# Performance work log

Hardware: AMD Instinct MI355X
Metric: run time of the kernel (lower is better)

The kernel has to match this reference:

```python
import jax, jax.numpy as jnp
import numpy as np

N = 50000
E = 800000
IN_DIM = 128
HID = 32
HEADS = 8
OUT_DIM = 2
NEG_SLOPE = 0.2


def setup_inputs() -> dict:
    key = jax.random.key(0)
    ks = jax.random.split(key, 10)
    x = jax.random.normal(ks[0], (N, IN_DIM), dtype=jnp.float32)
    edge_index = jax.random.randint(ks[1], (2, E), 0, N, dtype=jnp.int64)
    s = 0.1
    W1 = jax.random.normal(ks[2], (IN_DIM, HEADS * HID), dtype=jnp.float32) * s
    att_src1 = jax.random.normal(ks[3], (HEADS, HID), dtype=jnp.float32) * s
    att_dst1 = jax.random.normal(ks[4], (HEADS, HID), dtype=jnp.float32) * s
    b1 = jnp.zeros((HEADS * HID,), dtype=jnp.float32)
    W2 = jax.random.normal(ks[5], (HEADS * HID, OUT_DIM), dtype=jnp.float32) * s
    att_src2 = jax.random.normal(ks[6], (1, OUT_DIM), dtype=jnp.float32) * s
    att_dst2 = jax.random.normal(ks[7], (1, OUT_DIM), dtype=jnp.float32) * s
    b2 = jnp.zeros((OUT_DIM,), dtype=jnp.float32)
    return {"x": x, "edge_index": edge_index, "W1": W1, "att_src1": att_src1,
            "att_dst1": att_dst1, "b1": b1, "W2": W2, "att_src2": att_src2,
            "att_dst2": att_dst2, "b2": b2}


def gat_conv(x, src, dst, W, att_src, att_dst, bias, concat):
    # PyG GATConv (add_self_loops handled by caller already appended in src/dst)
    H, C = att_src.shape
    n = x.shape[0]
    h = (x @ W).reshape(n, H, C)                       # [N,H,C]
    a_src = jnp.einsum('nhc,hc->nh', h, att_src)       # [N,H]
    a_dst = jnp.einsum('nhc,hc->nh', h, att_dst)       # [N,H]
    e = jax.nn.leaky_relu(a_src[src] + a_dst[dst], NEG_SLOPE)  # [Etot,H]
    m = jax.lax.stop_gradient(jax.ops.segment_max(e, dst, num_segments=n))
    ee = jnp.exp(e - m[dst])
    denom = jax.ops.segment_sum(ee, dst, num_segments=n)
    alpha = ee / denom[dst]                            # segment softmax over incoming edges
    out = jax.ops.segment_sum(alpha[:, :, None] * h[src], dst, num_segments=n)  # [N,H,C]
    if concat:
        out = out.reshape(n, H * C)
    else:
        out = out.mean(axis=1)
    return out + bias


def reference(x, edge_index, W1, att_src1, att_dst1, b1, W2, att_src2, att_dst2, b2):
    n = x.shape[0]
    loop = jnp.arange(n, dtype=edge_index.dtype)
    src = jnp.concatenate([edge_index[0], loop])
    dst = jnp.concatenate([edge_index[1], loop])
    h = gat_conv(x, src, dst, W1, att_src1, att_dst1, b1, concat=True)
    h = jax.nn.elu(h)
    # dropout inactive in eval mode
    h = gat_conv(h, src, dst, W2, att_src2, att_dst2, b2, concat=False)
    return jax.nn.log_softmax(h, axis=1)
```

## Files before the change

### kernel.cpp

```cpp
#include <hip/hip_runtime.h>
#include <hip/hip_bf16.h>

#define NEG_SLOPE 0.2f
#define BSTRIDE 6144

typedef float f32x4 __attribute__((ext_vector_type(4)));
typedef short s16x4 __attribute__((ext_vector_type(4)));
typedef short bf16x8 __attribute__((ext_vector_type(8)));

__device__ __forceinline__ float lrelu(float x) { return x > 0.f ? x : NEG_SLOPE * x; }
__device__ __forceinline__ float bf2f(unsigned u) {
    return __uint_as_float(u << 16);
}
__device__ __forceinline__ unsigned short f2bf(float f) {
    unsigned int u = __float_as_uint(f);
    return (unsigned short)((u + 0x7FFF + ((u >> 16) & 1)) >> 16);
}

__device__ __forceinline__ int load_src(const int* ei, int E, int e, int is64) {
    return is64 ? ei[2 * (size_t)e] : ei[e];
}
__device__ __forceinline__ int load_dst(const int* ei, int E, int e, int is64) {
    return is64 ? ei[2 * (size_t)E + 2 * (size_t)e] : ei[(size_t)E + e];
}

__global__ void init2_kernel(const int* __restrict__ ei, int* __restrict__ flag,
                             int* __restrict__ bktCur) {
    int t = threadIdx.x;
    bktCur[t] = t * BSTRIDE;
    if (t == 0) {
        int z = 1;
        for (int k = 0; k < 64; ++k) if (ei[2 * k + 1] != 0) { z = 0; break; }
        *flag = z;
    }
}

__global__ __launch_bounds__(256) void bin_scatter(const int* __restrict__ ei, int E, int n,
                                                   const int* __restrict__ flag,
                                                   int* __restrict__ bktCur,
                                                   int* __restrict__ binned) {
    __shared__ int hist[256];
    __shared__ int gb[256];
    int t = threadIdx.x;
    hist[t] = 0;
    __syncthreads();
    int is64 = *flag;
    int base = blockIdx.x * 2048;
    int Etot = E + n;
    int rec[8], rb[8], rr[8];
#pragma unroll
    for (int k = 0; k < 8; ++k) {
        int e = base + k * 256 + t;
        rb[k] = -1;
        if (e < Etot) {
            int s, d;
            if (e < E) { s = load_src(ei, E, e, is64); d = load_dst(ei, E, e, is64); }
            else       { s = d = e - E; }
            int b = d >> 8;
            rb[k] = b;
            rec[k] = s | ((d & 255) << 24);
            rr[k] = atomicAdd(&hist[b], 1);
        }
    }
    __syncthreads();
    if (hist[t]) gb[t] = atomicAdd(&bktCur[t], hist[t]);
    __syncthreads();
#pragma unroll
    for (int k = 0; k < 8; ++k)
        if (rb[k] >= 0) binned[gb[rb[k]] + rr[k]] = rec[k];
}

__global__ __launch_bounds__(256) void bucket_build(const int* __restrict__ bktCur,
                                                    const int* __restrict__ binned,
                                                    int* __restrict__ offs,
                                                    int* __restrict__ degOut,
                                                    int* __restrict__ csr, int n) {
    __shared__ int deg[256];
    __shared__ int sd[256];
    int b = blockIdx.x;
    int t = threadIdx.x;
    int lo = b * BSTRIDE, hi = bktCur[b];
    deg[t] = 0;
    __syncthreads();
    for (int i = lo + t; i < hi; i += 256)
        atomicAdd(&deg[((unsigned)binned[i]) >> 24], 1);
    __syncthreads();
    int v = deg[t];
    sd[t] = v;
    __syncthreads();
    for (int o = 1; o < 256; o <<= 1) {
        int x = (t >= o) ? sd[t - o] : 0;
        __syncthreads();
        sd[t] += x;
        __syncthreads();
    }
    int excl = lo + sd[t] - v;
    int node = (b << 8) + t;
    if (node < n) { offs[node] = excl; degOut[node] = v; }
    __syncthreads();
    deg[t] = excl;
    __syncthreads();
    for (int i = lo + t; i < hi; i += 256) {
        unsigned r = (unsigned)binned[i];
        int pos = atomicAdd(&deg[r >> 24], 1);
        csr[pos] = (int)(r & 0xFFFFFF);
    }
}

__global__ __launch_bounds__(256) void w1prep_kernel(
        const float* __restrict__ W1, const float* __restrict__ att_src1,
        const float* __restrict__ att_dst1, unsigned short* __restrict__ w1t) {
    int t = threadIdx.x;
    if (blockIdx.x < 128) {
        int v = blockIdx.x * 256 + t;
        int col = v & 255, k = v >> 8;
        w1t[(size_t)col * 128 + k] = f2bf(W1[(size_t)k * 256 + col]);
    } else {
#pragma unroll
        for (int i = 0; i < 8; ++i) {
            int v = t + 256 * i;
            int j = v & 15, k = v >> 4;
            const float* av = (j < 8) ? att_src1 : att_dst1;
            int h = j & 7;
            float s = 0.f;
            for (int c = 0; c < 32; ++c)
                s += W1[(size_t)k * 256 + 32 * h + c] * av[h * 32 + c];
            w1t[(size_t)(256 + j) * 128 + k] = f2bf(s);
        }
    }
}

__device__ __forceinline__ bf16x8 read_frag(const char* base, int row, int kb) {
    int swz = (row & 7) << 4;
    const char* p = base + row * 256;
    s16x4 lo = *(const s16x4*)(p + (kb ^ swz));
    s16x4 hi = *(const s16x4*)(p + ((kb + 32) ^ swz));
    return __builtin_shufflevector(lo, hi, 0, 1, 2, 3, 4, 5, 6, 7);
}

__device__ __forceinline__ void load_px(const float* __restrict__ x, int m0, int n, int t,
                                        f32x4 (&px)[2][4]) {
#pragma unroll
    for (int q = 0; q < 2; ++q) {
        int u = t + 256 * q;
        int row = u >> 3, kseg = u & 7;
        int gr = m0 + row;
        bool ok = (u < 384) && (gr < n);
        const f32x4* p = (const f32x4*)(x + (size_t)gr * 128 + kseg * 16);
#pragma unroll
        for (int j = 0; j < 4; ++j) {
            f32x4 z = {0.f, 0.f, 0.f, 0.f};
            px[q][j] = ok ? p[j] : z;
        }
    }
}

#define XOFF 69632
__global__ __launch_bounds__(256, 2) void gemm1_kernel(
        const float* __restrict__ x, const unsigned short* __restrict__ w1t,
        unsigned short* __restrict__ h1u, float* __restrict__ asrc1,
        float* __restrict__ adst1, int n, int nchunk) {
    __shared__ __align__(16) char lds[81920];
    const int t = threadIdx.x;
    const int lane = t & 63, w = t >> 6;
    const int l15 = lane & 15, g = lane >> 4;

    for (int u = t; u < 4352; u += 256) {
        int col = u >> 4, seg = u & 15;
        int4 v = *(const int4*)(w1t + (size_t)col * 128 + seg * 8);
        *(int4*)(lds + col * 256 + ((seg * 16) ^ ((col & 7) << 4))) = v;
    }

    int c0 = blockIdx.x * 2;
    f32x4 px[2][4];
    load_px(x, c0 * 48, n, t, px);
    __syncthreads();

    bf16x8 Bf[4][5];
#pragma unroll
    for (int ks = 0; ks < 4; ++ks) {
#pragma unroll
        for (int nt = 0; nt < 5; ++nt) {
            if (nt < 4 || w == 0) {
                int col = (nt < 4) ? (64 * w + 16 * nt + l15) : (256 + l15);
                Bf[ks][nt] = read_frag(lds, col, 64 * ks + 8 * g);
            }
        }
    }

    for (int cc = 0; cc < 2; ++cc) {
        int chunk = c0 + cc;
        if (chunk >= nchunk) break;
        int m0 = chunk * 48;
#pragma unroll
        for (int q = 0; q < 2; ++q) {
            int u = t + 256 * q;
            if (u < 384) {
                int row = u >> 3, kseg = u & 7;
                union { unsigned short us[16]; int4 v[2]; } pk;
#pragma unroll
                for (int j = 0; j < 4; ++j)
#pragma unroll
                    for (int e = 0; e < 4; ++e) pk.us[j * 4 + e] = f2bf(px[q][j][e]);
                int base = XOFF + row * 256;
                int swz = (row & 7) << 4;
                *(int4*)(lds + base + ((kseg * 32) ^ swz)) = pk.v[0];
                *(int4*)(lds + base + ((kseg * 32 + 16) ^ swz)) = pk.v[1];
            }
        }
        __syncthreads();
        if (cc == 0) load_px(x, (c0 + 1) * 48, n, t, px);

        f32x4 acc[3][5];
#pragma unroll
        for (int mt = 0; mt < 3; ++mt)
#pragma unroll
            for (int nt = 0; nt < 5; ++nt)
#pragma unroll
                for (int r = 0; r < 4; ++r) acc[mt][nt][r] = 0.f;

#pragma unroll
        for (int ks = 0; ks < 4; ++ks) {
            bf16x8 Af[3];
#pragma unroll
            for (int mt = 0; mt < 3; ++mt)
                Af[mt] = read_frag(lds + XOFF, mt * 16 + l15, 64 * ks + 8 * g);
#pragma unroll
            for (int nt = 0; nt < 5; ++nt) {
                if (nt < 4 || w == 0) {
#pragma unroll
                    for (int mt = 0; mt < 3; ++mt)
                        acc[mt][nt] = __builtin_amdgcn_mfma_f32_16x16x32_bf16(
                            Af[mt], Bf[ks][nt], acc[mt][nt], 0, 0, 0);
                }
            }
        }

#pragma unroll
        for (int mt = 0; mt < 3; ++mt) {
#pragma unroll
            for (int r = 0; r < 4; ++r) {
                int row = m0 + 16 * mt + 4 * g + r;
                bool ok = row < n;
#pragma unroll
                for (int nt = 0; nt < 4; ++nt)
                    if (ok) h1u[(size_t)row * 256 + 64 * w + 16 * nt + l15] =
                        f2bf(acc[mt][nt][r]);
                if (w == 0 && ok) {
                    float v = acc[mt][4][r];
                    if (l15 < 8) asrc1[(size_t)row * 8 + l15] = v;
                    else         adst1[(size_t)row * 8 + (l15 - 8)] = v;
                }
            }
        }
        if (cc == 0) __syncthreads();
    }
}

__global__ __launch_bounds__(64) void aggregate_kernel(
        const int* __restrict__ offs, const int* __restrict__ deg,
        const int* __restrict__ csr,
        const float* __restrict__ asrc1, const float* __restrict__ adst1,
        const unsigned short* __restrict__ h1u, const float* __restrict__ b1,
        const float* __restrict__ W2, const float* __restrict__ att_src2,
        const float* __restrict__ att_dst2, float4* __restrict__ rec) {
    int d = blockIdx.x;
    int t = threadIdx.x;
    int h = t >> 3;
    int off = offs[d], end = off + deg[d];
    float ad = adst1[(size_t)d * 8 + h];
    float a0 = 0.f, a1 = 0.f, a2 = 0.f, a3 = 0.f, aw = 0.f;
    const unsigned short* hp = h1u + 4 * t;
    int i = off;
    for (; i + 8 <= end; i += 8) {
        int sIdx[8];
#pragma unroll
        for (int k = 0; k < 8; ++k) sIdx[k] = csr[i + k];
        float wv[8];
#pragma unroll
        for (int k = 0; k < 8; ++k)
            wv[k] = __expf(lrelu(asrc1[(size_t)sIdx[k] * 8 + h] + ad));
        ushort4 hv[8];
#pragma unroll
        for (int k = 0; k < 8; ++k)
            hv[k] = *(const ushort4*)(hp + (size_t)sIdx[k] * 256);
#pragma unroll
        for (int k = 0; k < 8; ++k) {
            a0 = fmaf(wv[k], bf2f(hv[k].x), a0);
            a1 = fmaf(wv[k], bf2f(hv[k].y), a1);
            a2 = fmaf(wv[k], bf2f(hv[k].z), a2);
            a3 = fmaf(wv[k], bf2f(hv[k].w), a3);
            aw += wv[k];
        }
    }
    for (; i < end; ++i) {
        int s = csr[i];
        float w = __expf(lrelu(asrc1[(size_t)s * 8 + h] + ad));
        ushort4 v = *(const ushort4*)(hp + (size_t)s * 256);
        a0 = fmaf(w, bf2f(v.x), a0); a1 = fmaf(w, bf2f(v.y), a1);
        a2 = fmaf(w, bf2f(v.z), a2); a3 = fmaf(w, bf2f(v.w), a3);
        aw += w;
    }
    float inv = 1.0f / aw;
    float4 bv = *(const float4*)(b1 + 4 * t);
    float v0 = fmaf(a0, inv, bv.x);
    float v1 = fmaf(a1, inv, bv.y);
    float v2 = fmaf(a2, inv, bv.z);
    float v3 = fmaf(a3, inv, bv.w);
    v0 = v0 > 0.f ? v0 : __expf(v0) - 1.f;
    v1 = v1 > 0.f ? v1 : __expf(v1) - 1.f;
    v2 = v2 > 0.f ? v2 : __expf(v2) - 1.f;
    v3 = v3 > 0.f ? v3 : __expf(v3) - 1.f;
    float4 w01 = *(const float4*)(W2 + 8 * t);
    float4 w23 = *(const float4*)(W2 + 8 * t + 4);
    float p0 = v0 * w01.x + v1 * w01.z + v2 * w23.x + v3 * w23.z;
    float p1 = v0 * w01.y + v1 * w01.w + v2 * w23.y + v3 * w23.w;
#pragma unroll
    for (int o = 32; o; o >>= 1) { p0 += __shfl_down(p0, o); p1 += __shfl_down(p1, o); }
    if (t == 0) {
        float s2a = att_src2[0], s2b = att_src2[1];
        float d2a = att_dst2[0], d2b = att_dst2[1];
        rec[d] = make_float4(p0, p1, p0 * s2a + p1 * s2b, p0 * d2a + p1 * d2b);
    }
}

__global__ __launch_bounds__(256) void layer2_kernel(
        const int* __restrict__ offs, const int* __restrict__ deg,
        const int* __restrict__ csr, const float4* __restrict__ rec,
        const float* __restrict__ b2, float* __restrict__ out, int n) {
    int t = threadIdx.x;
    int d = blockIdx.x * 16 + (t >> 4);
    if (d >= n) return;
    int li = t & 15;
    int off = offs[d], end = off + deg[d];
    float ad = rec[d].w;
    float se = 0.f, s0 = 0.f, s1 = 0.f;
    for (int i = off + li; i < end; i += 16) {
        int s = csr[i];
        float4 r = rec[s];
        float e = __expf(lrelu(r.z + ad));
        se += e;
        s0 = fmaf(e, r.x, s0);
        s1 = fmaf(e, r.y, s1);
    }
#pragma unroll
    for (int o = 8; o; o >>= 1) {
        se += __shfl_xor(se, o, 16);
        s0 += __shfl_xor(s0, o, 16);
        s1 += __shfl_xor(s1, o, 16);
    }
    if (li == 0) {
        float o0 = s0 / se + b2[0];
        float o1 = s1 / se + b2[1];
        float m2 = fmaxf(o0, o1);
        float lse = m2 + logf(__expf(o0 - m2) + __expf(o1 - m2));
        out[(size_t)d * 2 + 0] = o0 - lse;
        out[(size_t)d * 2 + 1] = o1 - lse;
    }
}

extern "C" void kernel_launch(void* const* d_in, const int* in_sizes, int n_in,
                              void* d_out, int out_size, void* d_ws, size_t ws_size,
                              hipStream_t stream) {
    const float* x        = (const float*)d_in[0];
    const int*   ei       = (const int*)d_in[1];
    const float* W1       = (const float*)d_in[2];
    const float* att_src1 = (const float*)d_in[3];
    const float* att_dst1 = (const float*)d_in[4];
    const float* b1       = (const float*)d_in[5];
    const float* W2       = (const float*)d_in[6];
    const float* att_src2 = (const float*)d_in[7];
    const float* att_dst2 = (const float*)d_in[8];
    const float* b2       = (const float*)d_in[9];
    float* out = (float*)d_out;

    int N = in_sizes[0] / 128;
    int E = in_sizes[1] / 2;
    int Etot = E + N;
    int NB = (N + 255) >> 8;
    int nbs = (Etot + 2047) / 2048;
    int nchunk = (N + 47) / 48;
    size_t binsz = (size_t)NB * BSTRIDE;

    char* W = (char*)d_ws;
    size_t o = 0;
    auto alloc = [&](size_t bytes) { size_t r = o; o = (o + bytes + 15) & ~(size_t)15; return r; };
    unsigned short* h1u  = (unsigned short*)(W + alloc((size_t)N * 256 * 2));
    float*  asrc1   = (float*)(W + alloc((size_t)N * 8 * 4));
    float*  adst1   = (float*)(W + alloc((size_t)N * 8 * 4));
    float4* rec     = (float4*)(W + alloc((size_t)N * 16));
    int*    offs    = (int*)(W + alloc((size_t)N * 4));
    int*    deg     = (int*)(W + alloc((size_t)N * 4));
    int*    bktCur  = (int*)(W + alloc(256 * 4));
    int*    flag    = (int*)(W + alloc(16));
    int*    csr     = (int*)(W + alloc(binsz * 4));
    int*    binned  = (int*)(W + alloc(binsz * 4));
    unsigned short* w1t = (unsigned short*)(W + alloc((size_t)272 * 128 * 2));

    init2_kernel<<<1, 256, 0, stream>>>(ei, flag, bktCur);
    bin_scatter<<<nbs, 256, 0, stream>>>(ei, E, N, flag, bktCur, binned);
    bucket_build<<<NB, 256, 0, stream>>>(bktCur, binned, offs, deg, csr, N);
    w1prep_kernel<<<129, 256, 0, stream>>>(W1, att_src1, att_dst1, w1t);
    gemm1_kernel<<<(nchunk + 1) / 2, 256, 0, stream>>>(x, w1t, h1u, asrc1, adst1, N, nchunk);
    aggregate_kernel<<<N, 64, 0, stream>>>(offs, deg, csr, asrc1, adst1, h1u, b1, W2,
                                           att_src2, att_dst2, rec);
    layer2_kernel<<<(N + 15) / 16, 256, 0, stream>>>(offs, deg, csr, rec, b2, out, N);
}
```

Before: 168.4 us.

## Stage GEMM1 output through swizzled LDS for coalesced stores; split aggregate launch

The GEMM1 epilogue now writes the bf16 results into a swizzled LDS tile, synchronises, and then emits 16-byte coalesced row stores to h1u instead of scattered 2-byte global stores. The attention-score writes move into a separate wave-0 loop. Edge-index loading in bin_scatter uses int2 reads for 64-bit indices. The aggregate kernel is also split into two half-size launches with a node offset. The extra barrier and LDS reuse add sync cost, and the split launch adds launch overhead with no obvious benefit.

```diff
diff --git a/kernel.cpp b/kernel.cpp
--- a/kernel.cpp
+++ b/kernel.cpp
@@ -15,13 +15,6 @@
 __device__ __forceinline__ unsigned short f2bf(float f) {
     unsigned int u = __float_as_uint(f);
     return (unsigned short)((u + 0x7FFF + ((u >> 16) & 1)) >> 16);
-}
-
-__device__ __forceinline__ int load_src(const int* ei, int E, int e, int is64) {
-    return is64 ? ei[2 * (size_t)e] : ei[e];
-}
-__device__ __forceinline__ int load_dst(const int* ei, int E, int e, int is64) {
-    return is64 ? ei[2 * (size_t)E + 2 * (size_t)e] : ei[(size_t)E + e];
 }
 
 __global__ void init2_kernel(const int* __restrict__ ei, int* __restrict__ flag,
@@ -54,8 +47,15 @@
         rb[k] = -1;
         if (e < Etot) {
             int s, d;
-            if (e < E) { s = load_src(ei, E, e, is64); d = load_dst(ei, E, e, is64); }
-            else       { s = d = e - E; }
+            if (e < E) {
+                if (is64) {
+                    s = ((const int2*)ei)[e].x;
+                    d = ((const int2*)(ei + 2 * (size_t)E))[e].x;
+                } else {
+                    s = ei[e];
+                    d = ei[(size_t)E + e];
+                }
+            } else { s = d = e - E; }
             int b = d >> 8;
             rb[k] = b;
             rec[k] = s | ((d & 255) << 24);
@@ -236,21 +236,41 @@
             }
         }
 
+        if (w == 0) {
+#pragma unroll
+            for (int mt = 0; mt < 3; ++mt)
+#pragma unroll
+                for (int r = 0; r < 4; ++r) {
+                    int row = m0 + 16 * mt + 4 * g + r;
+                    if (row < n) {
+                        float v = acc[mt][4][r];
+                        if (l15 < 8) asrc1[(size_t)row * 8 + l15] = v;
+                        else         adst1[(size_t)row * 8 + (l15 - 8)] = v;
+                    }
+                }
+        }
+
 #pragma unroll
         for (int mt = 0; mt < 3; ++mt) {
 #pragma unroll
             for (int r = 0; r < 4; ++r) {
-                int row = m0 + 16 * mt + 4 * g + r;
-                bool ok = row < n;
+                int lrow = 16 * mt + 4 * g + r;
+                int swz = (lrow & 7) << 4;
+                char* rp = lds + lrow * 512;
 #pragma unroll
                 for (int nt = 0; nt < 4; ++nt)
-                    if (ok) h1u[(size_t)row * 256 + 64 * w + 16 * nt + l15] =
+                    *(unsigned short*)(rp + ((2 * (64 * w + 16 * nt + l15)) ^ swz)) =
                         f2bf(acc[mt][nt][r]);
-                if (w == 0 && ok) {
-                    float v = acc[mt][4][r];
-                    if (l15 < 8) asrc1[(size_t)row * 8 + l15] = v;
-                    else         adst1[(size_t)row * 8 + (l15 - 8)] = v;
-                }
+            }
+        }
+        __syncthreads();
+        for (int v = t; v < 1536; v += 256) {
+            int lrow = v >> 5, seg = v & 31;
+            int row = m0 + lrow;
+            if (row < n) {
+                int swz = (lrow & 7) << 4;
+                int4 q = *(const int4*)(lds + lrow * 512 + ((seg * 16) ^ swz));
+                *(int4*)(h1u + (size_t)row * 256 + seg * 8) = q;
             }
         }
         if (cc == 0) __syncthreads();
@@ -263,8 +283,8 @@
         const float* __restrict__ asrc1, const float* __restrict__ adst1,
         const unsigned short* __restrict__ h1u, const float* __restrict__ b1,
         const float* __restrict__ W2, const float* __restrict__ att_src2,
-        const float* __restrict__ att_dst2, float4* __restrict__ rec) {
-    int d = blockIdx.x;
+        const float* __restrict__ att_dst2, float4* __restrict__ rec, int d0) {
+    int d = blockIdx.x + d0;
     int t = threadIdx.x;
     int h = t >> 3;
     int off = offs[d], end = off + deg[d];
@@ -381,6 +401,7 @@
     int nbs = (Etot + 2047) / 2048;
     int nchunk = (N + 47) / 48;
     size_t binsz = (size_t)NB * BSTRIDE;
+    int nh = N / 2;
 
     char* W = (char*)d_ws;
     size_t o = 0;
@@ -402,7 +423,9 @@
     bucket_build<<<NB, 256, 0, stream>>>(bktCur, binned, offs, deg, csr, N);
     w1prep_kernel<<<129, 256, 0, stream>>>(W1, att_src1, att_dst1, w1t);
     gemm1_kernel<<<(nchunk + 1) / 2, 256, 0, stream>>>(x, w1t, h1u, asrc1, adst1, N, nchunk);
-    aggregate_kernel<<<N, 64, 0, stream>>>(offs, deg, csr, asrc1, adst1, h1u, b1, W2,
-                                           att_src2, att_dst2, rec);
+    aggregate_kernel<<<nh, 64, 0, stream>>>(offs, deg, csr, asrc1, adst1, h1u, b1, W2,
+                                            att_src2, att_dst2, rec, 0);
+    aggregate_kernel<<<N - nh, 64, 0, stream>>>(offs, deg, csr, asrc1, adst1, h1u, b1, W2,
+                                                att_src2, att_dst2, rec, nh);
     layer2_kernel<<<(N + 15) / 16, 256, 0, stream>>>(offs, deg, csr, rec, b2, out, N);
 }
```

Result: slower. 175.2 us (+4.0%).
